# Performance work log

Measured on AMD Instinct MI355X. Metric: run time of the kernel, lower is better.

Reference implementation:

```python
import jax, jax.numpy as jnp
import numpy as np


def _rope_freqs(T, H, W, head_dim):
    # 3D RoPE frequency table, shape (T*H*W, head_dim)
    dim_t = head_dim - 4 * (head_dim // 6)
    dim_h = 2 * (head_dim // 6)
    dim_w = 2 * (head_dim // 6)
    base = 10000.0
    ft = 1.0 / base ** (np.arange(0, dim_t, 2)[: dim_t // 2].astype(np.float32) / dim_t)
    fh = 1.0 / base ** (np.arange(0, dim_h, 2)[: dim_h // 2].astype(np.float32) / dim_h)
    fw = 1.0 / base ** (np.arange(0, dim_w, 2)[: dim_w // 2].astype(np.float32) / dim_w)
    gt = np.arange(T, dtype=np.float32)
    gh = np.arange(H, dtype=np.float32)
    gw = np.arange(W, dtype=np.float32)
    # outer products, then repeat-interleave each freq twice: '... n -> ... (n r)', r=2
    Ft = np.repeat(gt[:, None] * ft[None, :], 2, axis=-1)  # [T, dim_t]
    Fh = np.repeat(gh[:, None] * fh[None, :], 2, axis=-1)  # [H, dim_h]
    Fw = np.repeat(gw[:, None] * fw[None, :], 2, axis=-1)  # [W, dim_w]
    Ft = np.broadcast_to(Ft[:, None, None, :], (T, H, W, Ft.shape[-1]))
    Fh = np.broadcast_to(Fh[None, :, None, :], (T, H, W, Fh.shape[-1]))
    Fw = np.broadcast_to(Fw[None, None, :, :], (T, H, W, Fw.shape[-1]))
    freqs = np.concatenate([Ft, Fh, Fw], axis=-1).reshape(T * H * W, head_dim)
    return jnp.asarray(freqs)


def _rotate_half(x):
    # pairs along last dim: (d r) with r=2 -> (-x2, x1)
    x = x.reshape(x.shape[:-1] + (x.shape[-1] // 2, 2))
    x1, x2 = x[..., 0], x[..., 1]
    return jnp.stack((-x2, x1), axis=-1).reshape(x.shape[:-2] + (-1,))


def _rms_norm(x, w, eps=1e-6):
    xf = x.astype(jnp.float32)
    y = xf * jax.lax.rsqrt(jnp.mean(xf * xf, axis=-1, keepdims=True) + eps)
    return y.astype(x.dtype) * w


def reference(x, qkv_w, qkv_b, q_norm_w, k_norm_w, proj_w, proj_b, t_size, h_size, w_size):
    B, N, C = x.shape
    Hn = 24
    D = C // Hn
    qkv = x @ qkv_w.T + qkv_b  # [B, N, 3C]
    qkv = qkv.reshape(B, N, 3, Hn, D).transpose(2, 0, 3, 1, 4)  # [3, B, H, N, D]
    q, k, v = qkv[0], qkv[1], qkv[2]
    q = _rms_norm(q, q_norm_w)
    k = _rms_norm(k, k_norm_w)
    # 3D RoPE
    freqs = _rope_freqs(int(t_size), int(h_size), int(w_size), D)  # [N, D]
    cos = jnp.cos(freqs)[None, None]  # [1,1,N,D]
    sin = jnp.sin(freqs)[None, None]
    qf, kf = q.astype(jnp.float32), k.astype(jnp.float32)
    q = (qf * cos + _rotate_half(qf) * sin).astype(q.dtype)
    k = (kf * cos + _rotate_half(kf) * sin).astype(k.dtype)
    # scaled dot-product attention
    scale = D ** -0.5
    scores = jnp.einsum('bhqd,bhkd->bhqk', q, k) * scale
    attn = jax.nn.softmax(scores, axis=-1)
    out = jnp.einsum('bhqk,bhkd->bhqd', attn, v)  # [B,H,N,D]
    out = out.transpose(0, 2, 1, 3).reshape(B, N, C)
    return out @ proj_w.T + proj_b


def setup_inputs() -> dict:
    key = jax.random.key(0)
    ks = jax.random.split(key, 6)
    B, N, C, D = 2, 2048, 3072, 128
    return {
        'x': jax.random.normal(ks[0], (B, N, C), jnp.float32),
        'qkv_w': jax.random.normal(ks[1], (3 * C, C), jnp.float32) * (C ** -0.5),
        'qkv_b': jax.random.normal(ks[2], (3 * C,), jnp.float32) * 0.02,
        'q_norm_w': jnp.ones((D,), jnp.float32),
        'k_norm_w': jnp.ones((D,), jnp.float32),
        'proj_w': jax.random.normal(ks[3], (C, C), jnp.float32) * (C ** -0.5),
        'proj_b': jax.random.normal(ks[4], (C,), jnp.float32) * 0.02,
        't_size': 8,
        'h_size': 16,
        'w_size': 16,
    }
```

## Files before the change

### kernel.cpp

```cpp
#include <hip/hip_runtime.h>
#include <math.h>

typedef __attribute__((ext_vector_type(8))) __bf16 bf16x8;
typedef __attribute__((ext_vector_type(4))) __bf16 bf16x4;
typedef __attribute__((ext_vector_type(2))) __bf16 bf16x2;
typedef __attribute__((ext_vector_type(4))) float f32x4;

#define MFMA16(a, b, c) __builtin_amdgcn_mfma_f32_16x16x32_bf16(a, b, c, 0, 0, 0)

typedef const __attribute__((address_space(1))) unsigned int* gas_t;
typedef __attribute__((address_space(3))) unsigned int* las_t;

__device__ __forceinline__ void g2lds16(const __bf16* g, __bf16* l) {
    __builtin_amdgcn_global_load_lds((gas_t)(const void*)g, (las_t)(void*)l, 16, 0, 0);
}

__global__ void pack_bf16(const float* __restrict__ src, __bf16* __restrict__ dst, int n4) {
    int idx = blockIdx.x * 256 + threadIdx.x;
    if (idx < n4) {
        float4 f = *(const float4*)(src + (size_t)idx * 4);
        bf16x4 o;
        o.x = (__bf16)f.x; o.y = (__bf16)f.y; o.z = (__bf16)f.z; o.w = (__bf16)f.w;
        *(bf16x4*)(dst + (size_t)idx * 4) = o;
    }
}


#define STAGE_A(bufi, hh, tt) do {                                                     \
    _Pragma("unroll")                                                                  \
    for (int l = 0; l < 2; ++l) {                                                      \
        int c = (l << 9) + tid, rh = c >> 3;                                           \
        int esw = ((c & 7) << 3) ^ ((rh & 7) << 3);                                    \
        int gm = m0 + ((rh >> 6) << 7) + ((hh) << 6) + (rh & 63);                      \
        g2lds16(A + (size_t)gm * K + ((tt) << 6) + esw, &As[bufi][hh][c << 3]);        \
    } } while (0)

#define STAGE_B(bufi, hh, tt) do {                                                     \
    _Pragma("unroll")                                                                  \
    for (int l = 0; l < 2; ++l) {                                                      \
        int c = (l << 9) + tid, rh = c >> 3;                                           \
        int esw = ((c & 7) << 3) ^ ((rh & 7) << 3);                                    \
        int gn = n0 + ((rh >> 5) << 6) + ((hh) << 5) + (rh & 31);                      \
        g2lds16(B + (size_t)gn * K + ((tt) << 6) + esw, &Bs[bufi][hh][c << 3]);        \
    } } while (0)

#define READ_A(bufi, hh) do {                                                          \
    _Pragma("unroll")                                                                  \
    for (int m2 = 0; m2 < 4; ++m2) {                                                   \
        _Pragma("unroll")                                                              \
        for (int kk = 0; kk < 2; ++kk)                                                 \
            af[m2][kk] = *(const bf16x8*)&As[bufi][hh][                                \
                (((wm << 6) + (m2 << 4) + lm) << 6) + (((kk << 5) + q8) ^ swz)];       \
    } } while (0)

#define READ_B(dst, bufi, hh) do {                                                     \
    _Pragma("unroll")                                                                  \
    for (int n2 = 0; n2 < 2; ++n2) {                                                   \
        _Pragma("unroll")                                                              \
        for (int kk = 0; kk < 2; ++kk)                                                 \
            dst[n2][kk] = *(const bf16x8*)&Bs[bufi][hh][                               \
                (((wn << 5) + (n2 << 4) + lm) << 6) + (((kk << 5) + q8) ^ swz)];       \
    } } while (0)

#define MMA_Q(mh, bvar, nh) do {                                                       \
    __builtin_amdgcn_s_setprio(1);                                                     \
    _Pragma("unroll")                                                                  \
    for (int m2 = 0; m2 < 4; ++m2) {                                                   \
        _Pragma("unroll")                                                              \
        for (int n2 = 0; n2 < 2; ++n2) {                                               \
            _Pragma("unroll")                                                          \
            for (int kk = 0; kk < 2; ++kk)                                             \
                acc[(mh) * 4 + m2][(nh) * 2 + n2] =                                    \
                    MFMA16(af[m2][kk], bvar[n2][kk], acc[(mh) * 4 + m2][(nh) * 2 + n2]); \
    } }                                                                                \
    __builtin_amdgcn_s_setprio(0); } while (0)

#define BAR __builtin_amdgcn_s_barrier()
#define MID do { BAR; asm volatile("s_waitcnt lgkmcnt(0)" ::: "memory"); } while (0)
#define VMW(n) asm volatile("s_waitcnt vmcnt(" #n ")" ::: "memory")
#define NOPS ((void)0)

#define TILE4(bufi, S1, S2, S3, S4, W4) do {                                           \
    READ_A(bufi, 0); READ_B(be, bufi, 0);                                              \
    S1; MID; MMA_Q(0, be, 0); BAR;                                                     \
    READ_B(bo, bufi, 1);                                                               \
    S2; MID; MMA_Q(0, bo, 1); BAR;                                                     \
    READ_A(bufi, 1);                                                                   \
    S3; MID; MMA_Q(1, bo, 1); BAR;                                                     \
    S4; W4; BAR; MMA_Q(1, be, 0); BAR; } while (0)

template <typename OutT>
__global__ __launch_bounds__(512, 2)
void gemm256_bt_bias(const __bf16* __restrict__ A, const __bf16* __restrict__ B,
                     const float* __restrict__ bias, OutT* __restrict__ C,
                     int M, int N, int K) {
    __shared__ __align__(16) __bf16 As[2][2][8192];
    __shared__ __align__(16) __bf16 Bs[2][2][8192];

    const int tid = threadIdx.x;
    const int lane = tid & 63, wave = tid >> 6;
    const int lm = lane & 15, quad = lane >> 4, q8 = quad << 3;
    const int wm = wave >> 2, wn = wave & 3;
    const int swz = (lm & 7) << 3;

    const int nwg = gridDim.x;
    const int wg = (blockIdx.x & 7) * (nwg >> 3) + (blockIdx.x >> 3);
    const int nbx = N >> 8;
    const int m0 = (wg / nbx) << 8;
    const int n0 = (wg % nbx) << 8;

    const int NT = K >> 6, ITER = NT >> 1;

    f32x4 acc[8][4] = {};
    bf16x8 af[4][2], be[2][2], bo[2][2];

    STAGE_A(0, 0, 0); STAGE_B(0, 0, 0); STAGE_B(0, 1, 0); STAGE_A(0, 1, 0);
    STAGE_A(1, 0, 1); STAGE_B(1, 0, 1); STAGE_B(1, 1, 1);
    VMW(6);
    BAR;

#pragma unroll 1
    for (int i = 0; i < ITER - 1; ++i) {
        const int b = 2 * i + 1, t2 = 2 * i + 2, t3 = 2 * i + 3;
        TILE4(0, STAGE_A(1, 1, b),  STAGE_A(0, 0, t2), STAGE_B(0, 0, t2), STAGE_B(0, 1, t2), VMW(6));
        TILE4(1, STAGE_A(0, 1, t2), STAGE_A(1, 0, t3), STAGE_B(1, 0, t3), STAGE_B(1, 1, t3), VMW(6));
    }
    {
        const int b = NT - 1;
        TILE4(0, STAGE_A(1, 1, b), NOPS, NOPS, NOPS, VMW(0));
        TILE4(1, NOPS, NOPS, NOPS, NOPS, NOPS);
    }

#pragma unroll
    for (int nf = 0; nf < 4; ++nf) {
        const int col = n0 + (wn << 6) + (nf << 4) + lm;
        const float bj = bias[col];
#pragma unroll
        for (int mf = 0; mf < 8; ++mf) {
            const int mb = m0 + (wm << 7) + (mf << 4) + (quad << 2);
#pragma unroll
            for (int r = 0; r < 4; ++r)
                C[(size_t)(mb + r) * N + col] = (OutT)(acc[mf][nf][r] + bj);
        }
    }
}

__global__ void rmsrope(__bf16* __restrict__ qkv, const float* __restrict__ qw,
                        const float* __restrict__ kw) {
    int bn = blockIdx.x;
    int n = bn & 2047;
    int tid = threadIdx.x, wave = tid >> 6, lane = tid & 63;
    int d0 = lane * 2;
    int t = n >> 8, hp = (n >> 4) & 15, wp = n & 15;
    float pos, fi;
    if (d0 < 44)      { pos = (float)t;  fi = (float)(d0 >> 1) * (2.0f / 44.0f); }
    else if (d0 < 86) { pos = (float)hp; fi = (float)((d0 - 44) >> 1) * (2.0f / 42.0f); }
    else              { pos = (float)wp; fi = (float)((d0 - 86) >> 1) * (2.0f / 42.0f); }
    float freq = expf(-fi * 9.210340371976184f);
    float ang = pos * freq, sn, cs;
    sincosf(ang, &sn, &cs);
    float w0q = qw[d0], w1q = qw[d0 + 1], w0k = kw[d0], w1k = kw[d0 + 1];

    for (int h = wave; h < 24; h += 4) {
        size_t base = (size_t)bn * 9216 + h * 128 + d0;
        {
            bf16x2 xv = *(bf16x2*)(qkv + base);
            float x0 = (float)xv.x, x1 = (float)xv.y;
            float ss = x0 * x0 + x1 * x1;
            for (int m = 1; m < 64; m <<= 1) ss += __shfl_xor(ss, m, 64);
            float rr = rsqrtf(ss * (1.0f / 128.0f) + 1e-6f);
            float y0 = x0 * rr * w0q, y1 = x1 * rr * w1q;
            bf16x2 st; st.x = (__bf16)(y0 * cs - y1 * sn); st.y = (__bf16)(y1 * cs + y0 * sn);
            *(bf16x2*)(qkv + base) = st;
        }
        {
            bf16x2 xv = *(bf16x2*)(qkv + base + 3072);
            float x0 = (float)xv.x, x1 = (float)xv.y;
            float ss = x0 * x0 + x1 * x1;
            for (int m = 1; m < 64; m <<= 1) ss += __shfl_xor(ss, m, 64);
            float rr = rsqrtf(ss * (1.0f / 128.0f) + 1e-6f);
            float y0 = x0 * rr * w0k, y1 = x1 * rr * w1k;
            bf16x2 st; st.x = (__bf16)(y0 * cs - y1 * sn); st.y = (__bf16)(y1 * cs + y0 * sn);
            *(bf16x2*)(qkv + base + 3072) = st;
        }
    }
}

__global__ __launch_bounds__(256, 2)
void flash(const __bf16* __restrict__ qkv, __bf16* __restrict__ Oo) {
    __shared__ __align__(16) __bf16 Ks[64 * 136];
    __shared__ __align__(16) __bf16 VTs[128 * 72];
    __shared__ __align__(16) __bf16 Ps[128 * 72];
    int bh = blockIdx.x >> 4, qt = blockIdx.x & 15;
    int b = bh / 24, h = bh % 24;
    int q0 = qt * 128;
    int tid = threadIdx.x, wave = tid >> 6, lane = tid & 63;
    int lm = lane & 15, q8 = (lane >> 4) * 8, quad = lane >> 4;
    int wb = wave * 32;
    const float sc = 0.08838834764831845f;

    bf16x8 qf[2][4];
    for (int i = 0; i < 2; ++i)
        for (int kk = 0; kk < 4; ++kk)
            qf[i][kk] = *(const bf16x8*)(qkv + (size_t)(b * 2048 + q0 + wb + i * 16 + lm) * 9216
                                         + h * 128 + kk * 32 + q8);

    float mrow[2] = {-__builtin_inff(), -__builtin_inff()};
    float lrow[2] = {0.f, 0.f};
    f32x4 oacc[2][8] = {};

    for (int nt = 0; nt < 32; ++nt) {
        int n0 = nt * 64;
        __syncthreads();
        for (int r = 0; r < 4; ++r) {
            int c = r * 256 + tid;
            int krow = c >> 4, kch = (c & 15) * 8;
            *(uint4*)(Ks + krow * 136 + kch) =
                *(const uint4*)(qkv + (size_t)(b * 2048 + n0 + krow) * 9216 + 3072 + h * 128 + kch);
            int vkey = c & 63, vch = (c >> 6) * 8;
            bf16x8 vv = *(const bf16x8*)(qkv + (size_t)(b * 2048 + n0 + vkey) * 9216 + 6144 + h * 128 + vch);
            for (int j = 0; j < 8; ++j)
                VTs[(vch + j) * 72 + vkey] = vv[j];
        }
        __syncthreads();

        f32x4 s[2][4] = {};
        for (int kk = 0; kk < 4; ++kk) {
            bf16x8 bk[4];
            for (int j = 0; j < 4; ++j)
                bk[j] = *(const bf16x8*)(Ks + (j * 16 + lm) * 136 + kk * 32 + q8);
            for (int i = 0; i < 2; ++i)
                for (int j = 0; j < 4; ++j)
                    s[i][j] = MFMA16(bk[j], qf[i][kk], s[i][j]);
        }
        for (int i = 0; i < 2; ++i) {
            float mx = -__builtin_inff();
            for (int j = 0; j < 4; ++j)
                for (int r = 0; r < 4; ++r)
                    mx = fmaxf(mx, s[i][j][r]);
            mx *= sc;
            mx = fmaxf(mx, __shfl_xor(mx, 16, 64));
            mx = fmaxf(mx, __shfl_xor(mx, 32, 64));
            float mn = fmaxf(mrow[i], mx);
            float alpha = __expf(mrow[i] - mn);
            mrow[i] = mn;
            float rs = 0.f;
            for (int j = 0; j < 4; ++j) {
                bf16x4 pw;
                for (int r = 0; r < 4; ++r) {
                    float p = __expf(s[i][j][r] * sc - mn);
                    rs += p;
                    pw[r] = (__bf16)p;
                }
                *(bf16x4*)(Ps + (wb + i * 16 + lm) * 72 + j * 16 + quad * 4) = pw;
            }
            rs += __shfl_xor(rs, 16, 64);
            rs += __shfl_xor(rs, 32, 64);
            lrow[i] = lrow[i] * alpha + rs;
            if (__any(alpha != 1.0f))
                for (int ct = 0; ct < 8; ++ct) oacc[i][ct] *= alpha;
        }
        for (int kk = 0; kk < 2; ++kk) {
            bf16x8 ap[2];
            for (int i = 0; i < 2; ++i)
                ap[i] = *(const bf16x8*)(Ps + (wb + i * 16 + lm) * 72 + kk * 32 + q8);
            for (int ct = 0; ct < 8; ++ct) {
                bf16x8 bv = *(const bf16x8*)(VTs + (ct * 16 + lm) * 72 + kk * 32 + q8);
                for (int i = 0; i < 2; ++i)
                    oacc[i][ct] = MFMA16(bv, ap[i], oacc[i][ct]);
            }
        }
    }
    for (int i = 0; i < 2; ++i) {
        float inv = 1.0f / lrow[i];
        int row = q0 + wb + i * 16 + lm;
        size_t base = ((size_t)b * 2048 + row) * 3072 + h * 128 + quad * 4;
        for (int ct = 0; ct < 8; ++ct) {
            bf16x4 ov;
            for (int r = 0; r < 4; ++r) ov[r] = (__bf16)(oacc[i][ct][r] * inv);
            *(bf16x4*)(Oo + base + ct * 16) = ov;
        }
    }
}

extern "C" void kernel_launch(void* const* d_in, const int* in_sizes, int n_in,
                              void* d_out, int out_size, void* d_ws, size_t ws_size,
                              hipStream_t stream) {
    const float* x      = (const float*)d_in[0];
    const float* qkv_w  = (const float*)d_in[1];
    const float* qkv_b  = (const float*)d_in[2];
    const float* qnw    = (const float*)d_in[3];
    const float* knw    = (const float*)d_in[4];
    const float* proj_w = (const float*)d_in[5];
    const float* proj_b = (const float*)d_in[6];
    float* out = (float*)d_out;
    char* ws = (char*)d_ws;

    __bf16* xb   = (__bf16*)(ws + 0);
    __bf16* attn = (__bf16*)(ws + 0);
    __bf16* w1b  = (__bf16*)(ws + 25165824);
    __bf16* w2b  = (__bf16*)(ws + 81788928);
    __bf16* qkvb = (__bf16*)(ws + 100663296);

    pack_bf16<<<12288, 256, 0, stream>>>(x, xb, 3145728);
    pack_bf16<<<27648, 256, 0, stream>>>(qkv_w, w1b, 7077888);
    pack_bf16<<<9216, 256, 0, stream>>>(proj_w, w2b, 2359296);

    gemm256_bt_bias<__bf16><<<576, 512, 0, stream>>>(xb, w1b, qkv_b, qkvb, 4096, 9216, 3072);

    rmsrope<<<4096, 256, 0, stream>>>(qkvb, qnw, knw);

    flash<<<768, 256, 0, stream>>>(qkvb, attn);

    gemm256_bt_bias<float><<<192, 512, 0, stream>>>(attn, w2b, proj_b, out, 4096, 3072, 3072);
}
```

Measured before the change: 823.2 us.

## Double-buffer LDS fragment registers to overlap reads with MFMA quadrants

Rewrites the GEMM main loop so that LDS fragment reads for the next MFMA quadrant are issued before the current quadrant's MFMAs, using two register sets each for A and B fragments. Partial lgkmcnt/vmcnt waits and sched_barrier fences control ordering, so LDS read latency and global-to-LDS staging are meant to hide behind matrix math. This costs more VGPRs under the 512-thread, 2-block launch bound, and the hand-tuned wait counts risk races if they are miscounted.

```diff
diff --git a/kernel.cpp b/kernel.cpp
--- a/kernel.cpp
+++ b/kernel.cpp
@@ -44,16 +44,16 @@
         g2lds16(B + (size_t)gn * K + ((tt) << 6) + esw, &Bs[bufi][hh][c << 3]);        \
     } } while (0)
 
-#define READ_A(bufi, hh) do {                                                          \
+#define READ_AH(dst, bufi, hh) do {                                                    \
     _Pragma("unroll")                                                                  \
     for (int m2 = 0; m2 < 4; ++m2) {                                                   \
         _Pragma("unroll")                                                              \
         for (int kk = 0; kk < 2; ++kk)                                                 \
-            af[m2][kk] = *(const bf16x8*)&As[bufi][hh][                                \
+            dst[m2][kk] = *(const bf16x8*)&As[bufi][hh][                               \
                 (((wm << 6) + (m2 << 4) + lm) << 6) + (((kk << 5) + q8) ^ swz)];       \
     } } while (0)
 
-#define READ_B(dst, bufi, hh) do {                                                     \
+#define READ_BH(dst, bufi, hh) do {                                                    \
     _Pragma("unroll")                                                                  \
     for (int n2 = 0; n2 < 2; ++n2) {                                                   \
         _Pragma("unroll")                                                              \
@@ -62,7 +62,7 @@
                 (((wn << 5) + (n2 << 4) + lm) << 6) + (((kk << 5) + q8) ^ swz)];       \
     } } while (0)
 
-#define MMA_Q(mh, bvar, nh) do {                                                       \
+#define MMA_Q(Aset, mh, Bset, nh) do {                                                 \
     __builtin_amdgcn_s_setprio(1);                                                     \
     _Pragma("unroll")                                                                  \
     for (int m2 = 0; m2 < 4; ++m2) {                                                   \
@@ -71,23 +71,14 @@
             _Pragma("unroll")                                                          \
             for (int kk = 0; kk < 2; ++kk)                                             \
                 acc[(mh) * 4 + m2][(nh) * 2 + n2] =                                    \
-                    MFMA16(af[m2][kk], bvar[n2][kk], acc[(mh) * 4 + m2][(nh) * 2 + n2]); \
+                    MFMA16(Aset[m2][kk], Bset[n2][kk], acc[(mh) * 4 + m2][(nh) * 2 + n2]); \
     } }                                                                                \
     __builtin_amdgcn_s_setprio(0); } while (0)
 
 #define BAR __builtin_amdgcn_s_barrier()
-#define MID do { BAR; asm volatile("s_waitcnt lgkmcnt(0)" ::: "memory"); } while (0)
+#define SCHEDB __builtin_amdgcn_sched_barrier(0)
+#define LGKM(n) asm volatile("s_waitcnt lgkmcnt(" #n ")" ::: "memory")
 #define VMW(n) asm volatile("s_waitcnt vmcnt(" #n ")" ::: "memory")
-#define NOPS ((void)0)
-
-#define TILE4(bufi, S1, S2, S3, S4, W4) do {                                           \
-    READ_A(bufi, 0); READ_B(be, bufi, 0);                                              \
-    S1; MID; MMA_Q(0, be, 0); BAR;                                                     \
-    READ_B(bo, bufi, 1);                                                               \
-    S2; MID; MMA_Q(0, bo, 1); BAR;                                                     \
-    READ_A(bufi, 1);                                                                   \
-    S3; MID; MMA_Q(1, bo, 1); BAR;                                                     \
-    S4; W4; BAR; MMA_Q(1, be, 0); BAR; } while (0)
 
 template <typename OutT>
 __global__ __launch_bounds__(512, 2)
@@ -112,23 +103,52 @@
     const int NT = K >> 6, ITER = NT >> 1;
 
     f32x4 acc[8][4] = {};
-    bf16x8 af[4][2], be[2][2], bo[2][2];
-
-    STAGE_A(0, 0, 0); STAGE_B(0, 0, 0); STAGE_B(0, 1, 0); STAGE_A(0, 1, 0);
-    STAGE_A(1, 0, 1); STAGE_B(1, 0, 1); STAGE_B(1, 1, 1);
-    VMW(6);
+    bf16x8 aA[4][2], aB[4][2], bA[2][2], bB[2][2];
+
+    STAGE_A(0, 0, 0); STAGE_B(0, 0, 0); STAGE_B(0, 1, 0);
+    STAGE_A(0, 1, 0); STAGE_A(1, 0, 1); STAGE_B(1, 0, 1); STAGE_B(1, 1, 1);
+    VMW(8);
     BAR;
+    READ_AH(aA, 0, 0); READ_BH(bA, 0, 0);
 
 #pragma unroll 1
     for (int i = 0; i < ITER - 1; ++i) {
         const int b = 2 * i + 1, t2 = 2 * i + 2, t3 = 2 * i + 3;
-        TILE4(0, STAGE_A(1, 1, b),  STAGE_A(0, 0, t2), STAGE_B(0, 0, t2), STAGE_B(0, 1, t2), VMW(6));
-        TILE4(1, STAGE_A(0, 1, t2), STAGE_A(1, 0, t3), STAGE_B(1, 0, t3), STAGE_B(1, 1, t3), VMW(6));
-    }
+        READ_BH(bB, 0, 1); STAGE_A(1, 1, b);  LGKM(4); BAR; SCHEDB;
+        MMA_Q(aA, 0, bA, 0); SCHEDB; VMW(8); BAR;
+        READ_AH(aB, 0, 1); STAGE_A(0, 0, t2); LGKM(8); BAR; SCHEDB;
+        MMA_Q(aA, 0, bB, 1); SCHEDB; VMW(8); BAR;
+        READ_AH(aA, 1, 0); STAGE_B(0, 0, t2); LGKM(8); BAR; SCHEDB;
+        MMA_Q(aB, 1, bB, 1); SCHEDB; VMW(8); BAR;
+        READ_BH(bB, 1, 0); STAGE_B(0, 1, t2);          BAR; SCHEDB;
+        MMA_Q(aB, 1, bA, 0); SCHEDB; VMW(8); BAR;
+        READ_BH(bA, 1, 1); STAGE_A(0, 1, t2); LGKM(4); BAR; SCHEDB;
+        MMA_Q(aA, 0, bB, 0); SCHEDB; VMW(8); BAR;
+        READ_AH(aB, 1, 1); STAGE_A(1, 0, t3); LGKM(8); BAR; SCHEDB;
+        MMA_Q(aA, 0, bA, 1); SCHEDB; VMW(8); BAR;
+        READ_AH(aA, 0, 0); STAGE_B(1, 0, t3); LGKM(8); BAR; SCHEDB;
+        MMA_Q(aB, 1, bA, 1); SCHEDB; VMW(8); BAR;
+        READ_BH(bA, 0, 0); STAGE_B(1, 1, t3);          BAR; SCHEDB;
+        MMA_Q(aB, 1, bB, 0); SCHEDB; VMW(8); BAR;
+    }
+
     {
         const int b = NT - 1;
-        TILE4(0, STAGE_A(1, 1, b), NOPS, NOPS, NOPS, VMW(0));
-        TILE4(1, NOPS, NOPS, NOPS, NOPS, NOPS);
+        READ_BH(bB, 0, 1); STAGE_A(1, 1, b); LGKM(4); BAR; SCHEDB;
+        MMA_Q(aA, 0, bA, 0); SCHEDB; VMW(8); BAR;
+        READ_AH(aB, 0, 1);                   LGKM(8); BAR; SCHEDB;
+        MMA_Q(aA, 0, bB, 1); SCHEDB; VMW(6); BAR;
+        READ_AH(aA, 1, 0);                   LGKM(8); BAR; SCHEDB;
+        MMA_Q(aB, 1, bB, 1); SCHEDB; VMW(4); BAR;
+        READ_BH(bB, 1, 0);                            BAR; SCHEDB;
+        MMA_Q(aB, 1, bA, 0); SCHEDB; VMW(2); BAR;
+        READ_BH(bA, 1, 1);                   LGKM(4); BAR; SCHEDB;
+        MMA_Q(aA, 0, bB, 0); SCHEDB; VMW(0); BAR;
+        READ_AH(aB, 1, 1);                   LGKM(8); BAR; SCHEDB;
+        MMA_Q(aA, 0, bA, 1); SCHEDB; BAR;
+        LGKM(0); SCHEDB;
+        MMA_Q(aB, 1, bA, 1); SCHEDB;
+        MMA_Q(aB, 1, bB, 0);
     }
 
 #pragma unroll
```

Result: slower. 1.262 ms (+53.3%).
